# Performance work log

Hardware: AMD Instinct MI355X
Metric: run time of the kernel (lower is better)

Reference implementation:

```python
import jax, jax.numpy as jnp
import numpy as np

B, T, V = 2, 1024, 50257
L, D, H, HKV = 8, 1024, 16, 4
HD = D // H          # 64 head dim
KVD = HKV * HD       # 256 kv projection dim
MLP = 4 * D          # 4096
BV, BD = 65536, 256  # bigram vocab / dim
VED = 128            # value-embedding dim


def _rms(x, eps=1e-6):
    return x * jax.lax.rsqrt(jnp.mean(x * x, axis=-1, keepdims=True) + eps)


def _rope_tables(seq_len, rd, base=10000.0, train_len=1024):
    # NTK base rescaling when seq_len > train_len (inactive here: T == train_len)
    if seq_len > train_len:
        base = base * (seq_len / train_len) ** (rd / (rd - 2))
    inv = 1.0 / base ** (np.arange(0, rd, 2, dtype=np.float32) / rd)
    fr = np.outer(np.arange(seq_len, dtype=np.float32), inv)
    cos = jnp.asarray(np.cos(fr), jnp.float32)[None, :, None, :]  # [1,T,1,rd/2]
    sin = jnp.asarray(np.sin(fr), jnp.float32)[None, :, None, :]
    return cos, sin


def _apply_rope(x, cos, sin):
    h = x.shape[-1] // 2
    x1, x2 = x[..., :h], x[..., h:]
    return jnp.concatenate([x1 * cos + x2 * sin, -x1 * sin + x2 * cos], axis=-1)


def _attn(xn, Wq, Wk, Wv, Wo, q_gain, v_embed, cos, sin):
    b, t, _ = xn.shape
    q = (xn @ Wq.T).reshape(b, t, H, HD)
    k = (xn @ Wk.T).reshape(b, t, HKV, HD)
    v = (xn @ Wv.T + v_embed).reshape(b, t, HKV, HD)
    q = _apply_rope(_rms(q), cos, sin) * q_gain[None, None, :, None]
    k = _apply_rope(_rms(k), cos, sin)
    G = H // HKV
    qg = q.reshape(b, t, HKV, G, HD)
    scores = jnp.einsum('bqhgd,bkhd->bhgqk', qg, k) / np.float32(np.sqrt(HD))
    mask = jnp.tril(jnp.ones((t, t), bool))
    scores = jnp.where(mask[None, None, None], scores, -jnp.inf)
    p = jax.nn.softmax(scores, axis=-1)
    yg = jnp.einsum('bhgqk,bkhd->bqhgd', p, v)  # [B,T,Hkv,G,HD]
    # xsa: reject component of each grouped head output along normalized v
    vnorm = jnp.sqrt(jnp.sum(v * v, axis=-1, keepdims=True))
    vn = (v / jnp.maximum(vnorm, 1e-12))[:, :, :, None, :]
    proj = jnp.sum(yg * vn, axis=-1, keepdims=True) * vn
    y = (yg - proj).reshape(b, t, D)
    return y @ Wo.T


def _mlp(xn, Wfc, Wp):
    h = xn @ Wfc.T
    h = jnp.where(h >= 0, h, 0.5 * h)  # leaky_relu(slope=0.5)
    return (h * h) @ Wp.T


def setup_inputs() -> dict:
    key = jax.random.key(0)
    ks = jax.random.split(key, 16)
    r = lambda i, shape, s: jax.random.normal(ks[i], shape, jnp.float32) * s
    return dict(
        token_ids=jax.random.randint(ks[0], (B, T), 0, V),
        embed_w=r(1, (V, D), 0.02),
        big_w=r(2, (BV, BD), 0.02),
        big_proj=r(3, (D, BD), 0.02),
        big_scale=jnp.float32(0.05),
        smear_gate=r(4, (D,), 0.02),
        ve_w=r(5, (V, VED), 0.01),
        ve_proj=r(6, (KVD, VED), 0.02),
        ve_scale=jnp.float32(0.1),
        Wq=r(7, (L, D, D), 0.02),
        Wk=r(8, (L, KVD, D), 0.02),
        Wv=r(9, (L, KVD, D), 0.02),
        Wo=r(10, (L, D, D), 0.02),
        q_gain=jnp.ones((L, H), jnp.float32),
        attn_scale=jnp.ones((L, D), jnp.float32),
        mlp_scale=jnp.ones((L, D), jnp.float32),
        resid_mix=jnp.tile(jnp.stack([jnp.ones(D), jnp.zeros(D)])[None], (L, 1, 1)).astype(jnp.float32),
        Wfc=r(11, (L, MLP, D), 0.02),
        Wp=r(12, (L, D, MLP), 0.02),
        head_w=r(13, (V, D), 0.02),
    )


def reference(token_ids, embed_w, big_w, big_proj, big_scale, smear_gate,
              ve_w, ve_proj, ve_scale, Wq, Wk, Wv, Wo, q_gain,
              attn_scale, mlp_scale, resid_mix, Wfc, Wp, head_w):
    ids = token_ids
    # bigram hash embedding
    t32 = ids.astype(jnp.int32)
    mod = jnp.int32(BV - 1)
    hsh = jnp.mod((36313 * t32[:, 1:]) ^ (27191 * t32[:, :-1]), mod)
    bg = jnp.concatenate([jnp.full((ids.shape[0], 1), mod, jnp.int32), hsh], axis=1)
    x = _rms(embed_w[ids]) + (big_w[bg] @ big_proj.T) * big_scale
    # smear gate: learned blend with previous token
    g = jax.nn.sigmoid(smear_gate)[None, None, :]
    x_prev = jnp.concatenate([jnp.zeros_like(x[:, :1]), x[:, :-1]], axis=1)
    x = (1 - g) * x + g * x_prev
    x0 = x
    v_embed = (ve_w[ids] @ ve_proj.T) * ve_scale  # [B,T,KVD]
    cos, sin = _rope_tables(T, HD)
    for l in range(L):
        mix = resid_mix[l]
        x_in = mix[0][None, None] * x + mix[1][None, None] * x0
        a = _attn(_rms(x_in), Wq[l], Wk[l], Wv[l], Wo[l], q_gain[l], v_embed, cos, sin)
        x = x_in + attn_scale[l][None, None] * a
        x = x + mlp_scale[l][None, None] * _mlp(_rms(x), Wfc[l], Wp[l])
    return _rms(x) @ head_w.T
```

## Files before the change

kernel.cpp:

```cpp
#include <hip/hip_runtime.h>
#include <hip/hip_bf16.h>

constexpr int Bc   = 2;
constexpr int Tc   = 1024;
constexpr int Vc   = 50257;
constexpr int Lc   = 8;
constexpr int Dc   = 1024;
constexpr int Hc   = 16;
constexpr int HKVc = 4;
constexpr int HDc  = 64;
constexpr int KVDc = 256;
constexpr int MLPc = 4096;
constexpr int BVc  = 65536;
constexpr int BDc  = 256;
constexpr int VEDc = 128;

constexpr int NTOK = Bc * Tc;
constexpr long SZ_X  = (long)NTOK * Dc;
constexpr long SZ_KV = (long)NTOK * KVDc;
constexpr long SZ_H  = (long)NTOK * MLPc;

constexpr int  VPAD = 50432;
constexpr long W_Q  = (long)Lc * Dc * Dc;
constexpr long W_KV = (long)Lc * KVDc * Dc;
// ... 133 lines not shown
    float* __restrict__ x, float* __restrict__ x0) {
  long idx = (long)blockIdx.x * 256 + threadIdx.x;
  if (idx >= SZ_X) return;
  int d = (int)(idx & (Dc - 1));
  int t = (int)((idx / Dc) & (Tc - 1));
  float g = 1.f / (1.f + expf(-gate[d]));
  float cur = raw[idx];
  float prev = (t > 0) ? raw[idx - Dc] : 0.f;
  float val = (1.f - g) * cur + g * prev;
  x[idx] = val;
  x0[idx] = val;
}

__device__ __forceinline__ void store_frag4(short* __restrict__ ph,
                                            short* __restrict__ pl, int bt,
                                            int d0, int K16, const float* v) {
  short4v h4, l4;
#pragma unroll
  for (int e = 0; e < 4; ++e) {
    short hb = f2bf(v[e]);
    h4[e] = hb;
    l4[e] = f2bf(v[e] - bf2f(hb));
  }
  int lanev = (bt & 31) + 32 * ((d0 >> 3) & 1);
  size_t off = (((size_t)(bt >> 5) * K16 + (d0 >> 4)) * 64 + lanev) * 8 + (d0 & 7);
  *(short4v*)(ph + off) = h4;
  *(short4v*)(pl + off) = l4;
}

__global__ __launch_bounds__(256) void prelayer_kernel(
    const float* __restrict__ x, const float* __restrict__ x0,
    const float* __restrict__ mix, float* __restrict__ x_in,
    short* __restrict__ xnh, short* __restrict__ xnl) {
  int bt = blockIdx.x;
  int tid = threadIdx.x;
  int d0 = tid * 4;
  const float* xr = x + (size_t)bt * Dc;
  const float* x0r = x0 + (size_t)bt * Dc;
  float4 xv = *(const float4*)(xr + d0);
  float4 x0v = *(const float4*)(x0r + d0);
  float4 m0 = *(const float4*)(mix + d0);
  float4 m1 = *(const float4*)(mix + Dc + d0);
  float vals[4] = {m0.x * xv.x + m1.x * x0v.x, m0.y * xv.y + m1.y * x0v.y,
                   m0.z * xv.z + m1.z * x0v.z, m0.w * xv.w + m1.w * x0v.w};
  float ss = vals[0] * vals[0] + vals[1] * vals[1] + vals[2] * vals[2] +
             vals[3] * vals[3];
  __shared__ float red[4];
  float wsum = wave_sum(ss);
  if ((tid & 63) == 0) red[tid >> 6] = wsum;
  __syncthreads();
  float tot = red[0] + red[1] + red[2] + red[3];
  float rn = rsqrtf(tot / (float)Dc + 1e-6f);
  *(float4*)(x_in + (size_t)bt * Dc + d0) =
      make_float4(vals[0], vals[1], vals[2], vals[3]);
  float vn[4] = {vals[0] * rn, vals[1] * rn, vals[2] * rn, vals[3] * rn};
  store_frag4(xnh, xnl, bt, d0, Dc >> 4, vn);
}

__global__ __launch_bounds__(256) void rms_split_kernel(
    const float* __restrict__ in, short* __restrict__ oh,
    short* __restrict__ ol) {
  int bt = blockIdx.x;
  int tid = threadIdx.x;
  int d0 = tid * 4;
  float4 v4 = *(const float4*)(in + (size_t)bt * Dc + d0);
  float v[4] = {v4.x, v4.y, v4.z, v4.w};
  float ss = v[0] * v[0] + v[1] * v[1] + v[2] * v[2] + v[3] * v[3];
  __shared__ float red[4];
  float wsum = wave_sum(ss);
  if ((tid & 63) == 0) red[tid >> 6] = wsum;
  __syncthreads();
  float tot = red[0] + red[1] + red[2] + red[3];
  float rn = rsqrtf(tot / (float)Dc + 1e-6f);
  float vn[4] = {v[0] * rn, v[1] * rn, v[2] * rn, v[3] * rn};
  store_frag4(oh, ol, bt, d0, Dc >> 4, vn);
}

template <int BM, int BN>
__device__ __forceinline__ void gemm_frag_core(
    const short* __restrict__ Afh, const short* __restrict__ Afl,
    const short* __restrict__ Bfh, const short* __restrict__ Bfl, int m0,
    int n0, int K, short* lds, floatx16 (*acc)[BN / 64]) {
  constexpr int RGA = BM / 32;
  constexpr int RGB = BN / 32;
  constexpr int SPW = RGA + RGB;
  constexpr int PLA = RGA * 1024;
  constexpr int PLB = RGB * 1024;
  constexpr int HB = 2 * (PLA + PLB);
  constexpr int FI = BM / 64;
  constexpr int FJ = BN / 64;

  int tid = threadIdx.x, lane = tid & 63, wv = tid >> 6;
  int K16 = K >> 4;

  const short* gsrc[SPW];
  int ldst[SPW];
#pragma unroll
  for (int t = 0; t < SPW; ++t) {
    int s = wv * SPW + t;
    const short* plane;
    int poff, rg, ks;
    size_t base;
    if (s < RGA * 4) {
      int p = s / (RGA * 2);
      int rem = s % (RGA * 2);
      rg = rem >> 1; ks = rem & 1;
      plane = p ? Afl : Afh;
      poff = p ? PLA : 0;
      base = (((size_t)(m0 >> 5) + rg) * K16 + ks) * 512;
    } else {
      int s2 = s - RGA * 4;
      int p = s2 / (RGB * 2);
      int rem = s2 % (RGB * 2);
      rg = rem >> 1; ks = rem & 1;
      plane = p ? Bfl : Bfh;
      poff = 2 * PLA + (p ? PLB : 0);
      base = (((size_t)(n0 >> 5) + rg) * K16 + ks) * 512;
    }
    gsrc[t] = plane + base + lane * 8;
    ldst[t] = poff + (rg * 2 + ks) * 512;
  }

  int wm = (wv >> 1) * (BM / 2), wn = (wv & 1) * (BN / 2);

#pragma unroll
  for (int t = 0; t < SPW; ++t) gll16(gsrc[t], lds + ldst[t]);
#pragma unroll
  for (int t = 0; t < SPW; ++t) gsrc[t] += 1024;
#pragma unroll
  for (int t = 0; t < SPW; ++t) gll16(gsrc[t], lds + HB + ldst[t]);
#pragma unroll
  for (int t = 0; t < SPW; ++t) gsrc[t] += 1024;

  int cur = 0;
  for (int k0 = 0; k0 < K; k0 += 32) {
    if (k0 + 32 < K) {
      if constexpr (SPW == 8) {
        asm volatile("s_waitcnt vmcnt(8)" ::: "memory");
      } else {
        asm volatile("s_waitcnt vmcnt(6)" ::: "memory");
      }
    } else {
      asm volatile("s_waitcnt vmcnt(0)" ::: "memory");
    }
    __builtin_amdgcn_s_barrier();
    __builtin_amdgcn_sched_barrier(0);

    const short* As_h = lds + cur * HB;
    const short* As_l = As_h + PLA;
    const short* Bs_h = As_h + 2 * PLA;
    const short* Bs_l = Bs_h + PLB;
    short8 ah[2][FI], alx[2][FI], bhx[2][FJ], blx[2][FJ];
#pragma unroll
    for (int ks = 0; ks < 2; ++ks) {
#pragma unroll
      for (int i = 0; i < FI; ++i) {
        int rg = (wm >> 5) + i;
        ah[ks][i]  = *(const short8*)(As_h + (rg * 2 + ks) * 512 + lane * 8);
        alx[ks][i] = *(const short8*)(As_l + (rg * 2 + ks) * 512 + lane * 8);
      }
#pragma unroll
      for (int j = 0; j < FJ; ++j) {
        int rg = (wn >> 5) + j;
        bhx[ks][j] = *(const short8*)(Bs_h + (rg * 2 + ks) * 512 + lane * 8);
        blx[ks][j] = *(const short8*)(Bs_l + (rg * 2 + ks) * 512 + lane * 8);
      }
    }
    asm volatile("s_waitcnt lgkmcnt(0)" ::: "memory");
    __builtin_amdgcn_sched_barrier(0);
    __builtin_amdgcn_s_barrier();

    if (k0 + 64 < K) {
#pragma unroll
      for (int t = 0; t < SPW; ++t) gll16(gsrc[t], lds + cur * HB + ldst[t]);
#pragma unroll
      for (int t = 0; t < SPW; ++t) gsrc[t] += 1024;
    }
    __builtin_amdgcn_sched_barrier(0);

    __builtin_amdgcn_s_setprio(1);
#pragma unroll
    for (int ks = 0; ks < 2; ++ks) {
#pragma unroll
      for (int i = 0; i < FI; ++i)
#pragma unroll
        for (int j = 0; j < FJ; ++j)
          acc[i][j] = __builtin_amdgcn_mfma_f32_32x32x16_bf16(ah[ks][i], bhx[ks][j], acc[i][j], 0, 0, 0);
#pragma unroll
      for (int i = 0; i < FI; ++i)
#pragma unroll
        for (int j = 0; j < FJ; ++j)
          acc[i][j] = __builtin_amdgcn_mfma_f32_32x32x16_bf16(ah[ks][i], blx[ks][j], acc[i][j], 0, 0, 0);
#pragma unroll
      for (int i = 0; i < FI; ++i)
#pragma unroll
        for (int j = 0; j < FJ; ++j)
          acc[i][j] = __builtin_amdgcn_mfma_f32_32x32x16_bf16(alx[ks][i], bhx[ks][j], acc[i][j], 0, 0, 0);
    }
    __builtin_amdgcn_s_setprio(0);
    cur ^= 1;
  }
}

__global__ __launch_bounds__(256, 2) void head_frag(
    const short* __restrict__ Afh, const short* __restrict__ Afl,
    const short* __restrict__ Bfh, const short* __restrict__ Bfl,
    float* __restrict__ C, int N, int K) {
  __shared__ short lds[32768];
  int bx = blockIdx.x, by = blockIdx.y;
  xcd_swizzle(bx, by, gridDim.x, gridDim.y);
  int m0 = bx * 128, n0 = by * 128;
  floatx16 acc[2][2] = {};
  gemm_frag_core<128, 128>(Afh, Afl, Bfh, Bfl, m0, n0, K, lds, acc);
  int lane = threadIdx.x & 63, wv = threadIdx.x >> 6;
  int wm = (wv >> 1) * 64, wn = (wv & 1) * 64;
  int cl = lane & 31, g2 = lane >> 5;
#pragma unroll
  for (int i = 0; i < 2; ++i)
#pragma unroll
    for (int j = 0; j < 2; ++j) {
      int col = n0 + wn + 32 * j + cl;
      if (col >= N) continue;
      floatx16 f = acc[i][j];
#pragma unroll
      for (int r = 0; r < 16; ++r) {
        int row = m0 + wm + 32 * i + (r & 3) + 8 * (r >> 2) + 4 * g2;
        C[(size_t)row * N + col] = f[r];
      }
    }
}

__global__ __launch_bounds__(256, 3) void wp_frag(
    const short* __restrict__ Afh, const short* __restrict__ Afl,
    const short* __restrict__ Bfh, const short* __restrict__ Bfl,
    float* __restrict__ C, const float* __restrict__ base,
    const float* __restrict__ colscale, int N, int K) {
  __shared__ short lds[24576];
  int bx = blockIdx.x, by = blockIdx.y;
  xcd_swizzle(bx, by, gridDim.x, gridDim.y);
  int m0 = bx * 64, n0 = by * 128;
  floatx16 acc[1][2] = {};
  gemm_frag_core<64, 128>(Afh, Afl, Bfh, Bfl, m0, n0, K, lds, acc);
  int lane = threadIdx.x & 63, wv = threadIdx.x >> 6;
  int wm = (wv >> 1) * 32, wn = (wv & 1) * 64;
  int cl = lane & 31, g2 = lane >> 5;
#pragma unroll
  for (int j = 0; j < 2; ++j) {
    int col = n0 + wn + 32 * j + cl;
    floatx16 f = acc[0][j];
    float cs = colscale ? colscale[col] : 1.f;
#pragma unroll
    for (int r = 0; r < 16; ++r) {
      int row = m0 + wm + (r & 3) + 8 * (r >> 2) + 4 * g2;
      size_t idx = (size_t)row * N + col;
      float v = f[r] * cs;
      if (base) v += base[idx];
      C[idx] = v;
    }
  }
}

__global__ __launch_bounds__(256, 3) void qkv_frag(
    const short* __restrict__ xnh, const short* __restrict__ xnl,
    const short* __restrict__ wqh, const short* __restrict__ wql,
    const short* __restrict__ wkh, const short* __restrict__ wkl,
    const short* __restrict__ wvh, const short* __restrict__ wvl,
    float* __restrict__ qb, float* __restrict__ kb, float* __restrict__ vb,
    const float* __restrict__ vemb, int K) {
  __shared__ short lds[24576];
  int bx = blockIdx.x, by = blockIdx.y;
  xcd_swizzle(bx, by, gridDim.x, gridDim.y);
  const short *Bh, *Bl;
  float* C;
  const float* base = nullptr;
  int n0, ldn;
  if (by < 8) {
    Bh = wqh; Bl = wql; C = qb; n0 = by * 128; ldn = Dc;
  } else if (by < 10) {
    Bh = wkh; Bl = wkl; C = kb; n0 = (by - 8) * 128; ldn = KVDc;
  } else {
    Bh = wvh; Bl = wvl; C = vb; base = vemb; n0 = (by - 10) * 128; ldn = KVDc;
  }
  int m0 = bx * 64;
  floatx16 acc[1][2] = {};
  gemm_frag_core<64, 128>(xnh, xnl, Bh, Bl, m0, n0, K, lds, acc);
  int lane = threadIdx.x & 63, wv = threadIdx.x >> 6;
  int wm = (wv >> 1) * 32, wn = (wv & 1) * 64;
  int cl = lane & 31, g2 = lane >> 5;
#pragma unroll
  for (int j = 0; j < 2; ++j) {
    int col = n0 + wn + 32 * j + cl;
    floatx16 f = acc[0][j];
#pragma unroll
    for (int r = 0; r < 16; ++r) {
      int row = m0 + wm + (r & 3) + 8 * (r >> 2) + 4 * g2;
      size_t idx = (size_t)row * ldn + col;
      float v = f[r];
      if (base) v += base[idx];
      C[idx] = v;
    }
  }
}

__global__ __launch_bounds__(256, 2) void fc_frag(
    const short* __restrict__ Afh, const short* __restrict__ Afl,
    const short* __restrict__ Bfh, const short* __restrict__ Bfl,
    short* __restrict__ Chf, short* __restrict__ Clf, int N, int K,
    int K16out) {
  __shared__ short lds[32768];
  int bx = blockIdx.x, by = blockIdx.y;
  xcd_swizzle(bx, by, gridDim.x, gridDim.y);
  int m0 = bx * 128, n0 = by * 128;
  floatx16 acc[2][2] = {};
  gemm_frag_core<128, 128>(Afh, Afl, Bfh, Bfl, m0, n0, K, lds, acc);
  int tid = threadIdx.x;
  int lane = tid & 63, wv = tid >> 6;
  int wm = (wv >> 1) * 64, wn = (wv & 1) * 64;
  int cl = lane & 31, g2 = lane >> 5;
  __syncthreads();
#pragma unroll
  for (int i = 0; i < 2; ++i)
#pragma unroll
    for (int j = 0; j < 2; ++j) {
      floatx16 f = acc[i][j];
#pragma unroll
      for (int r = 0; r < 16; ++r) {
        int rowl = wm + 32 * i + (r & 3) + 8 * (r >> 2) + 4 * g2;
        int coll = wn + 32 * j + cl;
        float v = f[r];
        float hx = (v >= 0.f) ? v : 0.5f * v;
        v = hx * hx;
        short hb = f2bf(v);
        short lb = f2bf(v - bf2f(hb));
        int sub = (rowl >> 5) * 8 + (coll >> 4);
        int lanev = (rowl & 31) + 32 * ((coll >> 3) & 1);
        int off = sub * 512 + lanev * 8 + (coll & 7);
        lds[off] = hb;
        lds[16384 + off] = lb;
      }
    }
  __syncthreads();
  size_t gbase = ((size_t)(m0 >> 5) * K16out + (n0 >> 4)) * 512;
#pragma unroll
  for (int u = 0; u < 8; ++u) {
    int idx = u * 2048 + tid * 8;
    int sub = idx >> 9, within = idx & 511;
    size_t gidx = gbase + ((size_t)(sub >> 3) * K16out + (sub & 7)) * 512 + within;
    *(short8*)(Chf + gidx) = *(const short8*)(lds + idx);
    *(short8*)(Clf + gidx) = *(const short8*)(lds + 16384 + idx);
  }
}

__global__ __launch_bounds__(256, 4) void gemm_bs64(
    const short* __restrict__ Ah, const short* __restrict__ Al,
    const short* __restrict__ Bfh, const short* __restrict__ Bfl,
    float* __restrict__ C, const float* __restrict__ base,
    const float* __restrict__ colscale, int N, int K) {
  __shared__ short lds[4096];
  int bx = blockIdx.x, by = blockIdx.y;
  xcd_swizzle(bx, by, gridDim.x, gridDim.y);
  int m0 = bx * 64, n0 = by * 128;
  constexpr int RGA = 2, SPW = 2, PLA = 2048, FI = 1, FJ = 2;
  int tid = threadIdx.x, lane = tid & 63, wv = tid >> 6;
  int K16 = K >> 4;
  const short* gsrc[SPW];
  int ldst[SPW];
#pragma unroll
  for (int t = 0; t < SPW; ++t) {
    int s = wv * SPW + t;
    int p = s / (RGA * 2);
    int rem = s % (RGA * 2);
    int rg = rem >> 1, ks = rem & 1;
    const short* plane = p ? Al : Ah;
    gsrc[t] = plane + (size_t)(m0 + rg * 32 + (lane & 31)) * K + ks * 16 +
              (lane >> 5) * 8;
    ldst[t] = p * PLA + (rg * 2 + ks) * 512;
  }
  int wm = (wv >> 1) * 32, wn = (wv & 1) * 64;
  const short* bbase_h[FJ];
  const short* bbase_l[FJ];
#pragma unroll
  for (int j = 0; j < FJ; ++j) {
    size_t rg = (size_t)((n0 + wn) >> 5) + j;
    bbase_h[j] = Bfh + rg * K16 * 512 + lane * 8;
    bbase_l[j] = Bfl + rg * K16 * 512 + lane * 8;
  }
  floatx16 acc[FI][FJ] = {};
  for (int k0 = 0; k0 < K; k0 += 32) {
#pragma unroll
    for (int t = 0; t < SPW; ++t) gll16(gsrc[t], lds + ldst[t]);
#pragma unroll
    for (int t = 0; t < SPW; ++t) gsrc[t] += 32;
    int ksg = k0 >> 4;
    short8 bh[2][FJ], bl2[2][FJ];
#pragma unroll
    for (int ks = 0; ks < 2; ++ks)
#pragma unroll
      for (int j = 0; j < FJ; ++j) {
        bh[ks][j]  = *(const short8*)(bbase_h[j] + (size_t)(ksg + ks) * 512);
        bl2[ks][j] = *(const short8*)(bbase_l[j] + (size_t)(ksg + ks) * 512);
      }
    __syncthreads();
    short8 ah[2][FI], alx[2][FI];
#pragma unroll
    for (int ks = 0; ks < 2; ++ks)
#pragma unroll
      for (int i = 0; i < FI; ++i) {
        int rg = (wm >> 5) + i;
        ah[ks][i]  = *(const short8*)(lds + (rg * 2 + ks) * 512 + lane * 8);
        alx[ks][i] = *(const short8*)(lds + PLA + (rg * 2 + ks) * 512 + lane * 8);
      }
    __builtin_amdgcn_s_setprio(1);
#pragma unroll
    for (int ks = 0; ks < 2; ++ks) {
#pragma unroll
      for (int i = 0; i < FI; ++i)
#pragma unroll
        for (int j = 0; j < FJ; ++j)
          acc[i][j] = __builtin_amdgcn_mfma_f32_32x32x16_bf16(ah[ks][i], bh[ks][j], acc[i][j], 0, 0, 0);
#pragma unroll
      for (int i = 0; i < FI; ++i)
#pragma unroll
        for (int j = 0; j < FJ; ++j)
          acc[i][j] = __builtin_amdgcn_mfma_f32_32x32x16_bf16(ah[ks][i], bl2[ks][j], acc[i][j], 0, 0, 0);
#pragma unroll
      for (int i = 0; i < FI; ++i)
#pragma unroll
        for (int j = 0; j < FJ; ++j)
          acc[i][j] = __builtin_amdgcn_mfma_f32_32x32x16_bf16(alx[ks][i], bh[ks][j], acc[i][j], 0, 0, 0);
    }
    __builtin_amdgcn_s_setprio(0);
    __syncthreads();
  }
  int cl = lane & 31, g2 = lane >> 5;
#pragma unroll
  for (int j = 0; j < FJ; ++j) {
    int col = n0 + wn + 32 * j + cl;
    floatx16 f = acc[0][j];
    float cs = colscale ? colscale[col] : 1.f;
#pragma unroll
    for (int r = 0; r < 16; ++r) {
      int row = m0 + wm + (r & 3) + 8 * (r >> 2) + 4 * g2;
      size_t idx = (size_t)row * N + col;
      float v = f[r] * cs;
      if (base) v += base[idx];
      C[idx] = v;
    }
  }
}

__global__ __launch_bounds__(256) void qkrope_kernel(
    float* __restrict__ q, float* __restrict__ k,
    const float* __restrict__ q_gain) {
  int bt = blockIdx.x;
  int t = bt % Tc;
  int tid = threadIdx.x;
  int lane = tid & 63, wv = tid >> 6;
  int fi = lane & 31;
  float inv = expf(-(float)(2 * fi) * (9.210340372f / 64.f));
  float ang = (float)t * inv;
  float cv = cosf(ang);
  float sv = sinf(ang);

#pragma unroll
  for (int hh = 0; hh < 4; ++hh) {
    int h = wv + hh * 4;
    float* qp = q + (size_t)bt * Dc + h * 64;
    float val = qp[lane];
    float ss = wave_sum(val * val);
    float rn = rsqrtf(ss / 64.f + 1e-6f);
    val *= rn;
    float partner = __shfl(val, lane ^ 32);
    float out = (lane < 32) ? (val * cv + partner * sv) : (val * cv - partner * sv);
    out *= q_gain[h];
    qp[lane] = out;
  }
  {
    int h = wv;
    float* kp = k + (size_t)bt * KVDc + h * 64;
    float val = kp[lane];
    float ss = wave_sum(val * val);
    float rn = rsqrtf(ss / 64.f + 1e-6f);
    val *= rn;
    float partner = __shfl(val, lane ^ 32);
    float out = (lane < 32) ? (val * cv + partner * sv) : (val * cv - partner * sv);
    kp[lane] = out;
  }
}

__global__ __launch_bounds__(256) void kvprep_kernel(
    const float* __restrict__ kb, const float* __restrict__ vb,
    short* __restrict__ khG, short* __restrict__ klG,
    short* __restrict__ vthG, short* __restrict__ vtlG) {
  __shared__ float kf[64][65];
  __shared__ float vf[64][65];
  int kt = blockIdx.x, bh = blockIdx.y;
  int b = bh >> 2, hkv = bh & 3;
  int tid = threadIdx.x;
#pragma unroll
  for (int u = 0; u < 4; ++u) {
    int idx = tid + u * 256;
    int row = idx >> 4, c4 = idx & 15;
    size_t off = ((size_t)(b * Tc + kt * 64 + row)) * KVDc + hkv * 64 + c4 * 4;
    float4 k4 = *(const float4*)(kb + off);
    float4 v4 = *(const float4*)(vb + off);
    kf[row][c4 * 4 + 0] = k4.x; kf[row][c4 * 4 + 1] = k4.y;
    kf[row][c4 * 4 + 2] = k4.z; kf[row][c4 * 4 + 3] = k4.w;
    vf[row][c4 * 4 + 0] = v4.x; vf[row][c4 * 4 + 1] = v4.y;
    vf[row][c4 * 4 + 2] = v4.z; vf[row][c4 * 4 + 3] = v4.w;
  }
  __syncthreads();
  size_t gb = ((size_t)(bh * (Tc / 64) + kt)) * 4096;
#pragma unroll
  for (int u = 0; u < 2; ++u) {
    int unit = tid + u * 256;
    int s = unit >> 6, p = unit & 63;
    {
      int half = s >> 2, rg = s & 3;
      int row = rg * 16 + (p & 15);
      int d0 = half * 32 + (p >> 4) * 8;
      short8 h8, l8;
#pragma unroll
      for (int e = 0; e < 8; ++e) {
        float v = kf[row][d0 + e];
        short hb = f2bf(v);
        h8[e] = hb;
        l8[e] = f2bf(v - bf2f(hb));
      }
      *(short8*)(khG + gb + s * 512 + p * 8) = h8;
      *(short8*)(klG + gb + s * 512 + p * 8) = l8;
    }
    {
      int ks = s >> 2, jd = s & 3;
// ... 99 lines not shown
      mx = fmaxf(mx, __shfl_xor(mx, 32));
      float m_new = fmaxf(m_run, mx);
      alv = __expf(m_run - m_new);
      float ts = 0.f;
#pragma unroll
      for (int i = 0; i < 4; ++i) {
#pragma unroll
        for (int r = 0; r < 4; ++r) {
          float p = __expf(st[i][r] - m_new);
          st[i][r] = p;
          ts += p;
        }
      }
      ts += __shfl_xor(ts, 16);
      ts += __shfl_xor(ts, 32);
      l_run = l_run * alv + ts;
      m_run = m_new;
    }

#pragma unroll
    for (int i = 0; i < 4; ++i) {
      short4v h4, l4;
#pragma unroll
      for (int r = 0; r < 4; ++r) {
        float p = st[i][r];
        short hb = f2bf(p);
        h4[r] = hb;
        l4[r] = f2bf(p - bf2f(hb));
      }
      int offp = (i >> 1) * 512 +
                 (x + (2 * (i & 1) + (g >> 1)) * 16) * 8 + 4 * (g & 1);
      *(short4v*)(PAhi + offp) = h4;
      *(short4v*)(PAlo + offp) = l4;
    }

#pragma unroll
    for (int r = 0; r < 4; ++r) {
      float a = __shfl(alv, 4 * g + r);
#pragma unroll
      for (int jd = 0; jd < 4; ++jd) o[jd][r] *= a;
    }
    __syncthreads();

#pragma unroll
    for (int ks = 0; ks < 2; ++ks) {
      short8 pa_h = *(const short8*)(PAhi + ks * 512 + lane * 8);
      short8 pa_l = *(const short8*)(PAlo + ks * 512 + lane * 8);
#pragma unroll
      for (int jd = 0; jd < 4; ++jd) {
        short8 vb_h = *(const short8*)(Vthi + ks * 2048 + jd * 512 + lane * 8);
        short8 vb_l = *(const short8*)(Vtlo + ks * 2048 + jd * 512 + lane * 8);
        o[jd] = __builtin_amdgcn_mfma_f32_16x16x32_bf16(pa_h, vb_h, o[jd], 0, 0, 0);
        o[jd] = __builtin_amdgcn_mfma_f32_16x16x32_bf16(pa_h, vb_l, o[jd], 0, 0, 0);
        o[jd] = __builtin_amdgcn_mfma_f32_16x16x32_bf16(pa_l, vb_h, o[jd], 0, 0, 0);
      }
    }
    __syncthreads();
  }

#pragma unroll
  for (int r = 0; r < 4; ++r) {
    float lr = __shfl(l_run, 4 * g + r);
    float rcp = 1.f / lr;
    int qrow = qbase + 4 * g + r;
    const float* vr = vg_ + ((size_t)(b * Tc + qrow)) * KVDc + hkv * 64;
    float vv[4], oo[4];
    float pn = 0.f, pd = 0.f;
#pragma unroll
    for (int jd = 0; jd < 4; ++jd) {
      vv[jd] = vr[16 * jd + x];
      oo[jd] = o[jd][r] * rcp;
      pn += vv[jd] * vv[jd];
      pd += oo[jd] * vv[jd];
    }
#pragma unroll
    for (int off = 1; off <= 8; off <<= 1) {
      pn += __shfl_xor(pn, off);
      pd += __shfl_xor(pd, off);
    }
    float nrm = sqrtf(pn);
    float mxv = fmaxf(nrm, 1e-12f);
    float si = 1.f / mxv;
    float co = pd * si * si;
    size_t ybase = ((size_t)(b * Tc + qrow)) * Dc + h * 64;
#pragma unroll
    for (int jd = 0; jd < 4; ++jd) {
      float val = oo[jd] - co * vv[jd];
      short hb = f2bf(val);
      yh_[ybase + 16 * jd + x] = hb;
      yl_[ybase + 16 * jd + x] = f2bf(val - bf2f(hb));
    }
  }
}

extern "C" void kernel_launch(void* const* d_in, const int* in_sizes, int n_in,
                              void* d_out, int out_size, void* d_ws,
                              size_t ws_size, hipStream_t stream) {
  const int* ids          = (const int*)d_in[0];
  const float* embed_w    = (const float*)d_in[1];
  const float* big_w      = (const float*)d_in[2];
  const float* big_proj   = (const float*)d_in[3];
  const float* big_scale  = (const float*)d_in[4];
  const float* smear_gate = (const float*)d_in[5];
  const float* ve_w       = (const float*)d_in[6];
  const float* ve_proj    = (const float*)d_in[7];
  const float* ve_scale   = (const float*)d_in[8];
  const float* Wq         = (const float*)d_in[9];
  const float* Wk         = (const float*)d_in[10];
  const float* Wv         = (const float*)d_in[11];
  const float* Wo         = (const float*)d_in[12];
  const float* q_gain     = (const float*)d_in[13];
  const float* attn_scale = (const float*)d_in[14];
  const float* mlp_scale  = (const float*)d_in[15];
  const float* resid_mix  = (const float*)d_in[16];
  const float* Wfc        = (const float*)d_in[17];
  const float* Wp         = (const float*)d_in[18];
  const float* head_w     = (const float*)d_in[19];
  float* out = (float*)d_out;

  char* p = (char*)d_ws;
  float* x     = (float*)p; p += SZ_X * 4;
  float* x0    = (float*)p; p += SZ_X * 4;
  float* x_in  = (float*)p; p += SZ_X * 4;
  float* qb    = (float*)p; p += SZ_X * 4;
  float* kb    = (float*)p; p += SZ_KV * 4;
  float* vb    = (float*)p; p += SZ_KV * 4;
  float* vemb  = (float*)p; p += SZ_KV * 4;
  float* raw_x = (float*)p; p += SZ_X * 4;
  short* xnh = (short*)p; p += SZ_X * 2;
  short* xnl = (short*)p; p += SZ_X * 2;
  short* yh  = (short*)p; p += SZ_X * 2;
  short* yl  = (short*)p; p += SZ_X * 2;
  short* hh  = (short*)p; p += SZ_H * 2;
  short* hl  = (short*)p; p += SZ_H * 2;
  short* khG  = (short*)p; p += SZ_KVP * 2;
  short* klG  = (short*)p; p += SZ_KVP * 2;
  short* vthG = (short*)p; p += SZ_KVP * 2;
  short* vtlG = (short*)p; p += SZ_KVP * 2;
  short* wqh = (short*)p; p += W_Q * 2;
  short* wql = (short*)p; p += W_Q * 2;
  short* wkh = (short*)p; p += W_KV * 2;
  short* wkl = (short*)p; p += W_KV * 2;
  short* wvh = (short*)p; p += W_KV * 2;
  short* wvl = (short*)p; p += W_KV * 2;
  short* woh = (short*)p; p += W_Q * 2;
  short* wol = (short*)p; p += W_Q * 2;
  short* wfh = (short*)p; p += W_FC * 2;
  short* wfl = (short*)p; p += W_FC * 2;
  short* wph = (short*)p; p += W_FC * 2;
  short* wpl = (short*)p; p += W_FC * 2;
  short* hwh = (short*)p; p += W_HD * 2;
  short* hwl = (short*)p; p += W_HD * 2;

  auto wcf = [&](const float* s, short* h, short* l2, int N, int Npad, int K) {
    long n8 = (long)Npad * (K >> 3);
    int blocks = (int)((n8 + 255) / 256);
    wcvt_frag_kernel<<<blocks, 256, 0, stream>>>(s, h, l2, N, Npad, K);
  };
  for (int l = 0; l < Lc; ++l) {
    wcf(Wq + (size_t)l * Dc * Dc, wqh + (size_t)l * Dc * Dc,
        wql + (size_t)l * Dc * Dc, Dc, Dc, Dc);
    wcf(Wk + (size_t)l * KVDc * Dc, wkh + (size_t)l * KVDc * Dc,
        wkl + (size_t)l * KVDc * Dc, KVDc, KVDc, Dc);
    wcf(Wv + (size_t)l * KVDc * Dc, wvh + (size_t)l * KVDc * Dc,
        wvl + (size_t)l * KVDc * Dc, KVDc, KVDc, Dc);
    wcf(Wo + (size_t)l * Dc * Dc, woh + (size_t)l * Dc * Dc,
        wol + (size_t)l * Dc * Dc, Dc, Dc, Dc);
    wcf(Wfc + (size_t)l * MLPc * Dc, wfh + (size_t)l * MLPc * Dc,
        wfl + (size_t)l * MLPc * Dc, MLPc, MLPc, Dc);
    wcf(Wp + (size_t)l * Dc * MLPc, wph + (size_t)l * Dc * MLPc,
        wpl + (size_t)l * Dc * MLPc, Dc, Dc, MLPc);
  }
  wcf(head_w, hwh, hwl, Vc, VPAD, Dc);

  embed_kernel<<<NTOK, 256, 0, stream>>>(ids, embed_w, big_w, big_proj,
                                         big_scale, ve_w, ve_proj, ve_scale,
                                         raw_x, vemb);
  smear_kernel<<<(int)(SZ_X / 256), 256, 0, stream>>>(raw_x, smear_gate, x, x0);

  for (int l = 0; l < Lc; ++l) {
    const float* mix = resid_mix + (size_t)l * 2 * Dc;
    prelayer_kernel<<<NTOK, 256, 0, stream>>>(x, x0, mix, x_in, xnh, xnl);
    qkv_frag<<<dim3(NTOK / 64, 12), 256, 0, stream>>>(
        xnh, xnl, wqh + (size_t)l * Dc * Dc, wql + (size_t)l * Dc * Dc,
        wkh + (size_t)l * KVDc * Dc, wkl + (size_t)l * KVDc * Dc,
        wvh + (size_t)l * KVDc * Dc, wvl + (size_t)l * KVDc * Dc, qb, kb, vb,
        vemb, Dc);
    qkrope_kernel<<<NTOK, 256, 0, stream>>>(qb, kb, q_gain + (size_t)l * Hc);
    kvprep_kernel<<<dim3(Tc / 64, Bc * HKVc), 256, 0, stream>>>(
        kb, vb, khG, klG, vthG, vtlG);
    attn_mfma<<<dim3(Bc * HKVc, Tc / 16), 256, 0, stream>>>(
        qb, vb, khG, klG, vthG, vtlG, yh, yl);
    gemm_bs64<<<dim3(NTOK / 64, Dc / 128), 256, 0, stream>>>(
        yh, yl, woh + (size_t)l * Dc * Dc, wol + (size_t)l * Dc * Dc, x, x_in,
        attn_scale + (size_t)l * Dc, Dc, Dc);
    rms_split_kernel<<<NTOK, 256, 0, stream>>>(x, xnh, xnl);
    fc_frag<<<dim3(NTOK / 128, MLPc / 128), 256, 0, stream>>>(
        xnh, xnl, wfh + (size_t)l * MLPc * Dc, wfl + (size_t)l * MLPc * Dc, hh,
        hl, MLPc, Dc, MLPc >> 4);
    wp_frag<<<dim3(NTOK / 64, Dc / 128), 256, 0, stream>>>(
        hh, hl, wph + (size_t)l * Dc * MLPc, wpl + (size_t)l * Dc * MLPc, x, x,
        mlp_scale + (size_t)l * Dc, Dc, MLPc);
  }

  rms_split_kernel<<<NTOK, 256, 0, stream>>>(x, xnh, xnl);
  head_frag<<<dim3(NTOK / 128, VPAD / 128), 256, 0, stream>>>(
      xnh, xnl, hwh, hwl, out, Vc, Dc);
}
```

Before: 4.416 ms.

## Load B fragments directly to registers and unify Wo GEMM into fragment kernel

The shared fragment GEMM core now stages only the A operand through LDS and loads the pre-fragmented B operand straight from global memory into registers, double-buffered across two unrolled K steps. LDS allocations shrink to match. The attention kernel now writes its output in the fragment layout, so the Wo projection can run through the common wp_frag kernel instead of the separate gemm_bs64. This cuts LDS traffic and footprint, which may allow more resident blocks, at the cost of more registers per thread and less reuse of B across waves.

```diff
diff --git a/kernel.cpp b/kernel.cpp
--- a/kernel.cpp
+++ b/kernel.cpp
@@ -239,13 +239,14 @@
     const short* __restrict__ Bfh, const short* __restrict__ Bfl, int m0,
     int n0, int K, short* lds, floatx16 (*acc)[BN / 64]) {
   constexpr int RGA = BM / 32;
-  constexpr int RGB = BN / 32;
-  constexpr int SPW = RGA + RGB;
+  constexpr int SPW = RGA;
   constexpr int PLA = RGA * 1024;
-  constexpr int PLB = RGB * 1024;
-  constexpr int HB = 2 * (PLA + PLB);
+  constexpr int HB = 2 * PLA;
   constexpr int FI = BM / 64;
   constexpr int FJ = BN / 64;
+  constexpr int NB = 4 * FJ;
+  constexpr int WT = RGA + NB;
+  static_assert(WT == 12 || WT == 10, "unexpected pipeline depth");
 
   int tid = threadIdx.x, lane = tid & 63, wv = tid >> 6;
   int K16 = K >> 4;
@@ -255,115 +256,126 @@
 #pragma unroll
   for (int t = 0; t < SPW; ++t) {
     int s = wv * SPW + t;
-    const short* plane;
-    int poff, rg, ks;
-    size_t base;
-    if (s < RGA * 4) {
-      int p = s / (RGA * 2);
-      int rem = s % (RGA * 2);
-      rg = rem >> 1; ks = rem & 1;
-      plane = p ? Afl : Afh;
-      poff = p ? PLA : 0;
-      base = (((size_t)(m0 >> 5) + rg) * K16 + ks) * 512;
-    } else {
-      int s2 = s - RGA * 4;
-      int p = s2 / (RGB * 2);
-      int rem = s2 % (RGB * 2);
-      rg = rem >> 1; ks = rem & 1;
-      plane = p ? Bfl : Bfh;
-      poff = 2 * PLA + (p ? PLB : 0);
-      base = (((size_t)(n0 >> 5) + rg) * K16 + ks) * 512;
-    }
-    gsrc[t] = plane + base + lane * 8;
-    ldst[t] = poff + (rg * 2 + ks) * 512;
+    int p = s / (RGA * 2);
+    int rem = s % (RGA * 2);
+    int rg = rem >> 1, ks = rem & 1;
+    const short* plane = p ? Afl : Afh;
+    gsrc[t] = plane + (((size_t)(m0 >> 5) + rg) * K16 + ks) * 512 + lane * 8;
+    ldst[t] = (p ? PLA : 0) + (rg * 2 + ks) * 512;
   }
 
   int wm = (wv >> 1) * (BM / 2), wn = (wv & 1) * (BN / 2);
 
+  const short* bph[2][FJ];
+  const short* bpl[2][FJ];
+#pragma unroll
+  for (int ks = 0; ks < 2; ++ks)
+#pragma unroll
+    for (int j = 0; j < FJ; ++j) {
+      size_t rgb = (size_t)((n0 + wn) >> 5) + j;
+      bph[ks][j] = Bfh + (rgb * K16 + ks) * 512 + lane * 8;
+      bpl[ks][j] = Bfl + (rgb * K16 + ks) * 512 + lane * 8;
+    }
+
+  short8 bh0[2][FJ], bl0[2][FJ], bh1[2][FJ], bl1[2][FJ];
+
 #pragma unroll
   for (int t = 0; t < SPW; ++t) gll16(gsrc[t], lds + ldst[t]);
 #pragma unroll
   for (int t = 0; t < SPW; ++t) gsrc[t] += 1024;
+  __builtin_amdgcn_sched_barrier(0);
+#pragma unroll
+  for (int ks = 0; ks < 2; ++ks)
+#pragma unroll
+    for (int j = 0; j < FJ; ++j) {
+      bh0[ks][j] = *(const short8*)(bph[ks][j]);
+      bl0[ks][j] = *(const short8*)(bpl[ks][j]);
+    }
+  __builtin_amdgcn_sched_barrier(0);
 #pragma unroll
   for (int t = 0; t < SPW; ++t) gll16(gsrc[t], lds + HB + ldst[t]);
 #pragma unroll
   for (int t = 0; t < SPW; ++t) gsrc[t] += 1024;
-
-  int cur = 0;
-  for (int k0 = 0; k0 < K; k0 += 32) {
-    if (k0 + 32 < K) {
-      if constexpr (SPW == 8) {
-        asm volatile("s_waitcnt vmcnt(8)" ::: "memory");
-      } else {
-        asm volatile("s_waitcnt vmcnt(6)" ::: "memory");
-      }
-    } else {
-      asm volatile("s_waitcnt vmcnt(0)" ::: "memory");
-    }
-    __builtin_amdgcn_s_barrier();
-    __builtin_amdgcn_sched_barrier(0);
-
-    const short* As_h = lds + cur * HB;
-    const short* As_l = As_h + PLA;
-    const short* Bs_h = As_h + 2 * PLA;
-    const short* Bs_l = Bs_h + PLB;
-    short8 ah[2][FI], alx[2][FI], bhx[2][FJ], blx[2][FJ];
-#pragma unroll
-    for (int ks = 0; ks < 2; ++ks) {
-#pragma unroll
-      for (int i = 0; i < FI; ++i) {
-        int rg = (wm >> 5) + i;
-        ah[ks][i]  = *(const short8*)(As_h + (rg * 2 + ks) * 512 + lane * 8);
-        alx[ks][i] = *(const short8*)(As_l + (rg * 2 + ks) * 512 + lane * 8);
-      }
-#pragma unroll
-      for (int j = 0; j < FJ; ++j) {
-        int rg = (wn >> 5) + j;
-        bhx[ks][j] = *(const short8*)(Bs_h + (rg * 2 + ks) * 512 + lane * 8);
-        blx[ks][j] = *(const short8*)(Bs_l + (rg * 2 + ks) * 512 + lane * 8);
-      }
-    }
-    asm volatile("s_waitcnt lgkmcnt(0)" ::: "memory");
-    __builtin_amdgcn_sched_barrier(0);
-    __builtin_amdgcn_s_barrier();
-
-    if (k0 + 64 < K) {
-#pragma unroll
-      for (int t = 0; t < SPW; ++t) gll16(gsrc[t], lds + cur * HB + ldst[t]);
-#pragma unroll
-      for (int t = 0; t < SPW; ++t) gsrc[t] += 1024;
-    }
-    __builtin_amdgcn_sched_barrier(0);
-
-    __builtin_amdgcn_s_setprio(1);
-#pragma unroll
-    for (int ks = 0; ks < 2; ++ks) {
-#pragma unroll
-      for (int i = 0; i < FI; ++i)
-#pragma unroll
-        for (int j = 0; j < FJ; ++j)
-          acc[i][j] = __builtin_amdgcn_mfma_f32_32x32x16_bf16(ah[ks][i], bhx[ks][j], acc[i][j], 0, 0, 0);
-#pragma unroll
-      for (int i = 0; i < FI; ++i)
-#pragma unroll
-        for (int j = 0; j < FJ; ++j)
-          acc[i][j] = __builtin_amdgcn_mfma_f32_32x32x16_bf16(ah[ks][i], blx[ks][j], acc[i][j], 0, 0, 0);
-#pragma unroll
-      for (int i = 0; i < FI; ++i)
-#pragma unroll
-        for (int j = 0; j < FJ; ++j)
-          acc[i][j] = __builtin_amdgcn_mfma_f32_32x32x16_bf16(alx[ks][i], bhx[ks][j], acc[i][j], 0, 0, 0);
-    }
-    __builtin_amdgcn_s_setprio(0);
-    cur ^= 1;
-  }
+  __builtin_amdgcn_sched_barrier(0);
+#pragma unroll
+  for (int ks = 0; ks < 2; ++ks)
+#pragma unroll
+    for (int j = 0; j < FJ; ++j) {
+      bh1[ks][j] = *(const short8*)(bph[ks][j] + 1024);
+      bl1[ks][j] = *(const short8*)(bpl[ks][j] + 1024);
+    }
+  __builtin_amdgcn_sched_barrier(0);
+
+#define FRAG_STEP(BUFOFF, BH, BL, LAST, ISS, SNEXT)                            \
+  do {                                                                         \
+    if (LAST) {                                                                \
+      asm volatile("s_waitcnt vmcnt(0)" ::: "memory");                         \
+    } else if constexpr (WT == 12) {                                           \
+      asm volatile("s_waitcnt vmcnt(12)" ::: "memory");                        \
+    } else {                                                                   \
+      asm volatile("s_waitcnt vmcnt(10)" ::: "memory");                        \
+    }                                                                          \
+    __builtin_amdgcn_s_barrier();                                              \
+    __builtin_amdgcn_sched_barrier(0);                                         \
+    const short* As_h_ = lds + (BUFOFF);                                       \
+    const short* As_l_ = As_h_ + PLA;                                          \
+    short8 ah_[2][FI], al_[2][FI];                                             \
+    _Pragma("unroll") for (int ks = 0; ks < 2; ++ks)                           \
+        _Pragma("unroll") for (int i = 0; i < FI; ++i) {                       \
+      int rg_ = (wm >> 5) + i;                                                 \
+      ah_[ks][i] = *(const short8*)(As_h_ + (rg_ * 2 + ks) * 512 + lane * 8);  \
+      al_[ks][i] = *(const short8*)(As_l_ + (rg_ * 2 + ks) * 512 + lane * 8);  \
+    }                                                                          \
+    asm volatile("s_waitcnt lgkmcnt(0)" ::: "memory");                         \
+    __builtin_amdgcn_sched_barrier(0);                                         \
+    __builtin_amdgcn_s_barrier();                                              \
+    if (ISS) {                                                                 \
+      _Pragma("unroll") for (int t = 0; t < SPW; ++t)                          \
+          gll16(gsrc[t], lds + (BUFOFF) + ldst[t]);                            \
+      _Pragma("unroll") for (int t = 0; t < SPW; ++t) gsrc[t] += 1024;         \
+    }                                                                          \
+    __builtin_amdgcn_sched_barrier(0);                                         \
+    __builtin_amdgcn_s_setprio(1);                                             \
+    _Pragma("unroll") for (int ks = 0; ks < 2; ++ks) {                         \
+      _Pragma("unroll") for (int i = 0; i < FI; ++i)                           \
+          _Pragma("unroll") for (int j = 0; j < FJ; ++j) acc[i][j] =           \
+          __builtin_amdgcn_mfma_f32_32x32x16_bf16(ah_[ks][i], BH[ks][j],       \
+                                                  acc[i][j], 0, 0, 0);         \
+      _Pragma("unroll") for (int i = 0; i < FI; ++i)                           \
+          _Pragma("unroll") for (int j = 0; j < FJ; ++j) acc[i][j] =           \
+          __builtin_amdgcn_mfma_f32_32x32x16_bf16(ah_[ks][i], BL[ks][j],       \
+                                                  acc[i][j], 0, 0, 0);         \
+      _Pragma("unroll") for (int i = 0; i < FI; ++i)                           \
+          _Pragma("unroll") for (int j = 0; j < FJ; ++j) acc[i][j] =           \
+          __builtin_amdgcn_mfma_f32_32x32x16_bf16(al_[ks][i], BH[ks][j],       \
+                                                  acc[i][j], 0, 0, 0);         \
+    }                                                                          \
+    __builtin_amdgcn_s_setprio(0);                                             \
+    __builtin_amdgcn_sched_barrier(0);                                         \
+    if (ISS) {                                                                 \
+      size_t so_ = (size_t)(SNEXT) * 1024;                                     \
+      _Pragma("unroll") for (int ks = 0; ks < 2; ++ks)                         \
+          _Pragma("unroll") for (int j = 0; j < FJ; ++j) {                     \
+        BH[ks][j] = *(const short8*)(bph[ks][j] + so_);                        \
+        BL[ks][j] = *(const short8*)(bpl[ks][j] + so_);                        \
+      }                                                                        \
+    }                                                                          \
+    __builtin_amdgcn_sched_barrier(0);                                         \
+  } while (0)
+
+  int nsteps = K >> 5;
+  for (int s = 0; s < nsteps; s += 2) {
+    FRAG_STEP(0, bh0, bl0, false, (s + 2 < nsteps), s + 2);
+    FRAG_STEP(HB, bh1, bl1, (s + 2 >= nsteps), (s + 3 < nsteps), s + 3);
+  }
+#undef FRAG_STEP
 }
 
 __global__ __launch_bounds__(256, 2) void head_frag(
     const short* __restrict__ Afh, const short* __restrict__ Afl,
     const short* __restrict__ Bfh, const short* __restrict__ Bfl,
     float* __restrict__ C, int N, int K) {
-  __shared__ short lds[32768];
+  __shared__ short lds[16384];
   int bx = blockIdx.x, by = blockIdx.y;
   xcd_swizzle(bx, by, gridDim.x, gridDim.y);
   int m0 = bx * 128, n0 = by * 128;
@@ -392,7 +404,7 @@
     const short* __restrict__ Bfh, const short* __restrict__ Bfl,
     float* __restrict__ C, const float* __restrict__ base,
     const float* __restrict__ colscale, int N, int K) {
-  __shared__ short lds[24576];
+  __shared__ short lds[8192];
   int bx = blockIdx.x, by = blockIdx.y;
   xcd_swizzle(bx, by, gridDim.x, gridDim.y);
   int m0 = bx * 64, n0 = by * 128;
@@ -424,7 +436,7 @@
     const short* __restrict__ wvh, const short* __restrict__ wvl,
     float* __restrict__ qb, float* __restrict__ kb, float* __restrict__ vb,
     const float* __restrict__ vemb, int K) {
-  __shared__ short lds[24576];
+  __shared__ short lds[8192];
   int bx = blockIdx.x, by = blockIdx.y;
   xcd_swizzle(bx, by, gridDim.x, gridDim.y);
   const short *Bh, *Bl;
@@ -508,104 +520,6 @@
   }
 }
 
-__global__ __launch_bounds__(256, 4) void gemm_bs64(
-    const short* __restrict__ Ah, const short* __restrict__ Al,
-    const short* __restrict__ Bfh, const short* __restrict__ Bfl,
-    float* __restrict__ C, const float* __restrict__ base,
-    const float* __restrict__ colscale, int N, int K) {
-  __shared__ short lds[4096];
-  int bx = blockIdx.x, by = blockIdx.y;
-  xcd_swizzle(bx, by, gridDim.x, gridDim.y);
-  int m0 = bx * 64, n0 = by * 128;
-  constexpr int RGA = 2, SPW = 2, PLA = 2048, FI = 1, FJ = 2;
-  int tid = threadIdx.x, lane = tid & 63, wv = tid >> 6;
-  int K16 = K >> 4;
-  const short* gsrc[SPW];
-  int ldst[SPW];
-#pragma unroll
-  for (int t = 0; t < SPW; ++t) {
-    int s = wv * SPW + t;
-    int p = s / (RGA * 2);
-    int rem = s % (RGA * 2);
-    int rg = rem >> 1, ks = rem & 1;
-    const short* plane = p ? Al : Ah;
-    gsrc[t] = plane + (size_t)(m0 + rg * 32 + (lane & 31)) * K + ks * 16 +
-              (lane >> 5) * 8;
-    ldst[t] = p * PLA + (rg * 2 + ks) * 512;
-  }
-  int wm = (wv >> 1) * 32, wn = (wv & 1) * 64;
-  const short* bbase_h[FJ];
-  const short* bbase_l[FJ];
-#pragma unroll
-  for (int j = 0; j < FJ; ++j) {
-    size_t rg = (size_t)((n0 + wn) >> 5) + j;
-    bbase_h[j] = Bfh + rg * K16 * 512 + lane * 8;
-    bbase_l[j] = Bfl + rg * K16 * 512 + lane * 8;
-  }
-  floatx16 acc[FI][FJ] = {};
-  for (int k0 = 0; k0 < K; k0 += 32) {
-#pragma unroll
-    for (int t = 0; t < SPW; ++t) gll16(gsrc[t], lds + ldst[t]);
-#pragma unroll
-    for (int t = 0; t < SPW; ++t) gsrc[t] += 32;
-    int ksg = k0 >> 4;
-    short8 bh[2][FJ], bl2[2][FJ];
-#pragma unroll
-    for (int ks = 0; ks < 2; ++ks)
-#pragma unroll
-      for (int j = 0; j < FJ; ++j) {
-        bh[ks][j]  = *(const short8*)(bbase_h[j] + (size_t)(ksg + ks) * 512);
-        bl2[ks][j] = *(const short8*)(bbase_l[j] + (size_t)(ksg + ks) * 512);
-      }
-    __syncthreads();
-    short8 ah[2][FI], alx[2][FI];
-#pragma unroll
-    for (int ks = 0; ks < 2; ++ks)
-#pragma unroll
-      for (int i = 0; i < FI; ++i) {
-        int rg = (wm >> 5) + i;
-        ah[ks][i]  = *(const short8*)(lds + (rg * 2 + ks) * 512 + lane * 8);
-        alx[ks][i] = *(const short8*)(lds + PLA + (rg * 2 + ks) * 512 + lane * 8);
-      }
-    __builtin_amdgcn_s_setprio(1);
-#pragma unroll
-    for (int ks = 0; ks < 2; ++ks) {
-#pragma unroll
-      for (int i = 0; i < FI; ++i)
-#pragma unroll
-        for (int j = 0; j < FJ; ++j)
-          acc[i][j] = __builtin_amdgcn_mfma_f32_32x32x16_bf16(ah[ks][i], bh[ks][j], acc[i][j], 0, 0, 0);
-#pragma unroll
-      for (int i = 0; i < FI; ++i)
-#pragma unroll
-        for (int j = 0; j < FJ; ++j)
-          acc[i][j] = __builtin_amdgcn_mfma_f32_32x32x16_bf16(ah[ks][i], bl2[ks][j], acc[i][j], 0, 0, 0);
-#pragma unroll
-      for (int i = 0; i < FI; ++i)
-#pragma unroll
-        for (int j = 0; j < FJ; ++j)
-          acc[i][j] = __builtin_amdgcn_mfma_f32_32x32x16_bf16(alx[ks][i], bh[ks][j], acc[i][j], 0, 0, 0);
-    }
-    __builtin_amdgcn_s_setprio(0);
-    __syncthreads();
-  }
-  int cl = lane & 31, g2 = lane >> 5;
-#pragma unroll
-  for (int j = 0; j < FJ; ++j) {
-    int col = n0 + wn + 32 * j + cl;
-    floatx16 f = acc[0][j];
-    float cs = colscale ? colscale[col] : 1.f;
-#pragma unroll
-    for (int r = 0; r < 16; ++r) {
-      int row = m0 + wm + (r & 3) + 8 * (r >> 2) + 4 * g2;
-      size_t idx = (size_t)row * N + col;
-      float v = f[r] * cs;
-      if (base) v += base[idx];
-      C[idx] = v;
-    }
-  }
-}
-
 __global__ __launch_bounds__(256) void qkrope_kernel(
     float* __restrict__ q, float* __restrict__ k,
     const float* __restrict__ q_gain) {
@@ -871,13 +785,16 @@
     float mxv = fmaxf(nrm, 1e-12f);
     float si = 1.f / mxv;
     float co = pd * si * si;
-    size_t ybase = ((size_t)(b * Tc + qrow)) * Dc + h * 64;
+    int grow = b * Tc + qrow;
+    size_t fb = ((size_t)(grow >> 5)) * 64 * 512 +
+                ((size_t)(grow & 31) + 32 * (x >> 3)) * 8 + (x & 7);
 #pragma unroll
     for (int jd = 0; jd < 4; ++jd) {
       float val = oo[jd] - co * vv[jd];
       short hb = f2bf(val);
-      yh_[ybase + 16 * jd + x] = hb;
-      yl_[ybase + 16 * jd + x] = f2bf(val - bf2f(hb));
+      size_t off = fb + (size_t)(h * 4 + jd) * 512;
+      yh_[off] = hb;
+      yl_[off] = f2bf(val - bf2f(hb));
     }
   }
 }
@@ -980,7 +897,7 @@
         kb, vb, khG, klG, vthG, vtlG);
     attn_mfma<<<dim3(Bc * HKVc, Tc / 16), 256, 0, stream>>>(
         qb, vb, khG, klG, vthG, vtlG, yh, yl);
-    gemm_bs64<<<dim3(NTOK / 64, Dc / 128), 256, 0, stream>>>(
+    wp_frag<<<dim3(NTOK / 64, Dc / 128), 256, 0, stream>>>(
         yh, yl, woh + (size_t)l * Dc * Dc, wol + (size_t)l * Dc * Dc, x, x_in,
         attn_scale + (size_t)l * Dc, Dc, Dc);
     rms_split_kernel<<<NTOK, 256, 0, stream>>>(x, xnh, xnl);
```

Result: slower. 4.691 ms (+6.2%).

## Write attention output in fragment layout and reuse wp_frag for Wo projection

Applied to the files above, without the earlier changes.

The attention kernel now stores its bf16 hi/lo output straight into the pre-swizzled fragment layout used by wp_frag. That lets the Wo projection run through wp_frag instead of gemm_bs64, which staged A tiles through LDS, and gemm_bs64 is removed. Per-layer weight conversion launches are also merged into one launch per weight type across all layers, which cuts launch overhead. This is correct only if the fragment indexing matches wp_frag's layout at K=1024 and the frag layout of stacked layers lines up with the per-layer offsets.

```diff
diff --git a/kernel.cpp b/kernel.cpp
--- a/kernel.cpp
+++ b/kernel.cpp
@@ -508,104 +508,6 @@
   }
 }
 
-__global__ __launch_bounds__(256, 4) void gemm_bs64(
-    const short* __restrict__ Ah, const short* __restrict__ Al,
-    const short* __restrict__ Bfh, const short* __restrict__ Bfl,
-    float* __restrict__ C, const float* __restrict__ base,
-    const float* __restrict__ colscale, int N, int K) {
-  __shared__ short lds[4096];
-  int bx = blockIdx.x, by = blockIdx.y;
-  xcd_swizzle(bx, by, gridDim.x, gridDim.y);
-  int m0 = bx * 64, n0 = by * 128;
-  constexpr int RGA = 2, SPW = 2, PLA = 2048, FI = 1, FJ = 2;
-  int tid = threadIdx.x, lane = tid & 63, wv = tid >> 6;
-  int K16 = K >> 4;
-  const short* gsrc[SPW];
-  int ldst[SPW];
-#pragma unroll
-  for (int t = 0; t < SPW; ++t) {
-    int s = wv * SPW + t;
-    int p = s / (RGA * 2);
-    int rem = s % (RGA * 2);
-    int rg = rem >> 1, ks = rem & 1;
-    const short* plane = p ? Al : Ah;
-    gsrc[t] = plane + (size_t)(m0 + rg * 32 + (lane & 31)) * K + ks * 16 +
-              (lane >> 5) * 8;
-    ldst[t] = p * PLA + (rg * 2 + ks) * 512;
-  }
-  int wm = (wv >> 1) * 32, wn = (wv & 1) * 64;
-  const short* bbase_h[FJ];
-  const short* bbase_l[FJ];
-#pragma unroll
-  for (int j = 0; j < FJ; ++j) {
-    size_t rg = (size_t)((n0 + wn) >> 5) + j;
-    bbase_h[j] = Bfh + rg * K16 * 512 + lane * 8;
-    bbase_l[j] = Bfl + rg * K16 * 512 + lane * 8;
-  }
-  floatx16 acc[FI][FJ] = {};
-  for (int k0 = 0; k0 < K; k0 += 32) {
-#pragma unroll
-    for (int t = 0; t < SPW; ++t) gll16(gsrc[t], lds + ldst[t]);
-#pragma unroll
-    for (int t = 0; t < SPW; ++t) gsrc[t] += 32;
-    int ksg = k0 >> 4;
-    short8 bh[2][FJ], bl2[2][FJ];
-#pragma unroll
-    for (int ks = 0; ks < 2; ++ks)
-#pragma unroll
-      for (int j = 0; j < FJ; ++j) {
-        bh[ks][j]  = *(const short8*)(bbase_h[j] + (size_t)(ksg + ks) * 512);
-        bl2[ks][j] = *(const short8*)(bbase_l[j] + (size_t)(ksg + ks) * 512);
-      }
-    __syncthreads();
-    short8 ah[2][FI], alx[2][FI];
-#pragma unroll
-    for (int ks = 0; ks < 2; ++ks)
-#pragma unroll
-      for (int i = 0; i < FI; ++i) {
-        int rg = (wm >> 5) + i;
-        ah[ks][i]  = *(const short8*)(lds + (rg * 2 + ks) * 512 + lane * 8);
-        alx[ks][i] = *(const short8*)(lds + PLA + (rg * 2 + ks) * 512 + lane * 8);
-      }
-    __builtin_amdgcn_s_setprio(1);
-#pragma unroll
-    for (int ks = 0; ks < 2; ++ks) {
-#pragma unroll
-      for (int i = 0; i < FI; ++i)
-#pragma unroll
-        for (int j = 0; j < FJ; ++j)
-          acc[i][j] = __builtin_amdgcn_mfma_f32_32x32x16_bf16(ah[ks][i], bh[ks][j], acc[i][j], 0, 0, 0);
-#pragma unroll
-      for (int i = 0; i < FI; ++i)
-#pragma unroll
-        for (int j = 0; j < FJ; ++j)
-          acc[i][j] = __builtin_amdgcn_mfma_f32_32x32x16_bf16(ah[ks][i], bl2[ks][j], acc[i][j], 0, 0, 0);
-#pragma unroll
-      for (int i = 0; i < FI; ++i)
-#pragma unroll
-        for (int j = 0; j < FJ; ++j)
-          acc[i][j] = __builtin_amdgcn_mfma_f32_32x32x16_bf16(alx[ks][i], bh[ks][j], acc[i][j], 0, 0, 0);
-    }
-    __builtin_amdgcn_s_setprio(0);
-    __syncthreads();
-  }
-  int cl = lane & 31, g2 = lane >> 5;
-#pragma unroll
-  for (int j = 0; j < FJ; ++j) {
-    int col = n0 + wn + 32 * j + cl;
-    floatx16 f = acc[0][j];
-    float cs = colscale ? colscale[col] : 1.f;
-#pragma unroll
-    for (int r = 0; r < 16; ++r) {
-      int row = m0 + wm + (r & 3) + 8 * (r >> 2) + 4 * g2;
-      size_t idx = (size_t)row * N + col;
-      float v = f[r] * cs;
-      if (base) v += base[idx];
-      C[idx] = v;
-    }
-  }
-}
-
 __global__ __launch_bounds__(256) void qkrope_kernel(
     float* __restrict__ q, float* __restrict__ k,
     const float* __restrict__ q_gain) {
@@ -871,13 +773,16 @@
     float mxv = fmaxf(nrm, 1e-12f);
     float si = 1.f / mxv;
     float co = pd * si * si;
-    size_t ybase = ((size_t)(b * Tc + qrow)) * Dc + h * 64;
+    int grow = b * Tc + qrow;
+    size_t fb = ((size_t)(grow >> 5)) * 64 * 512 +
+                ((size_t)(grow & 31) + 32 * (x >> 3)) * 8 + (x & 7);
 #pragma unroll
     for (int jd = 0; jd < 4; ++jd) {
       float val = oo[jd] - co * vv[jd];
       short hb = f2bf(val);
-      yh_[ybase + 16 * jd + x] = hb;
-      yl_[ybase + 16 * jd + x] = f2bf(val - bf2f(hb));
+      size_t off = fb + (size_t)(h * 4 + jd) * 512;
+      yh_[off] = hb;
+      yl_[off] = f2bf(val - bf2f(hb));
     }
   }
 }
@@ -946,20 +851,12 @@
     int blocks = (int)((n8 + 255) / 256);
     wcvt_frag_kernel<<<blocks, 256, 0, stream>>>(s, h, l2, N, Npad, K);
   };
-  for (int l = 0; l < Lc; ++l) {
-    wcf(Wq + (size_t)l * Dc * Dc, wqh + (size_t)l * Dc * Dc,
-        wql + (size_t)l * Dc * Dc, Dc, Dc, Dc);
-    wcf(Wk + (size_t)l * KVDc * Dc, wkh + (size_t)l * KVDc * Dc,
-        wkl + (size_t)l * KVDc * Dc, KVDc, KVDc, Dc);
-    wcf(Wv + (size_t)l * KVDc * Dc, wvh + (size_t)l * KVDc * Dc,
-        wvl + (size_t)l * KVDc * Dc, KVDc, KVDc, Dc);
-    wcf(Wo + (size_t)l * Dc * Dc, woh + (size_t)l * Dc * Dc,
-        wol + (size_t)l * Dc * Dc, Dc, Dc, Dc);
-    wcf(Wfc + (size_t)l * MLPc * Dc, wfh + (size_t)l * MLPc * Dc,
-        wfl + (size_t)l * MLPc * Dc, MLPc, MLPc, Dc);
-    wcf(Wp + (size_t)l * Dc * MLPc, wph + (size_t)l * Dc * MLPc,
-        wpl + (size_t)l * Dc * MLPc, Dc, Dc, MLPc);
-  }
+  wcf(Wq, wqh, wql, Lc * Dc, Lc * Dc, Dc);
+  wcf(Wk, wkh, wkl, Lc * KVDc, Lc * KVDc, Dc);
+  wcf(Wv, wvh, wvl, Lc * KVDc, Lc * KVDc, Dc);
+  wcf(Wo, woh, wol, Lc * Dc, Lc * Dc, Dc);
+  wcf(Wfc, wfh, wfl, Lc * MLPc, Lc * MLPc, Dc);
+  wcf(Wp, wph, wpl, Lc * Dc, Lc * Dc, MLPc);
   wcf(head_w, hwh, hwl, Vc, VPAD, Dc);
 
   embed_kernel<<<NTOK, 256, 0, stream>>>(ids, embed_w, big_w, big_proj,
@@ -980,7 +877,7 @@
         kb, vb, khG, klG, vthG, vtlG);
     attn_mfma<<<dim3(Bc * HKVc, Tc / 16), 256, 0, stream>>>(
         qb, vb, khG, klG, vthG, vtlG, yh, yl);
-    gemm_bs64<<<dim3(NTOK / 64, Dc / 128), 256, 0, stream>>>(
+    wp_frag<<<dim3(NTOK / 64, Dc / 128), 256, 0, stream>>>(
         yh, yl, woh + (size_t)l * Dc * Dc, wol + (size_t)l * Dc * Dc, x, x_in,
         attn_scale + (size_t)l * Dc, Dc, Dc);
     rms_split_kernel<<<NTOK, 256, 0, stream>>>(x, xnh, xnl);
```

New measurement: 4.265 ms (median of 2 runs). -3.4%, faster.
